# Optimization experiments

Measured on AMD Instinct MI355X. Metric: run time of the kernel, lower is better.

Reference implementation:

```python
import jax, jax.numpy as jnp
import numpy as np

N_USERS = 1_000_000
AVG_DEG = 32
E = N_USERS * AVG_DEG
K = 5
IN_F = 1
OUT_F = 64
BN_EPS = 1e-5


def setup_inputs() -> dict:
    key = jax.random.key(0)
    ks = jax.random.split(key, 6)
    stdv = 1.0 / np.sqrt(IN_F * K)
    return {
        "x": jax.random.normal(ks[0], (N_USERS, IN_F), dtype=jnp.float32),
        "edge_index": jax.random.randint(ks[1], (2, E), 0, N_USERS, dtype=jnp.int32),
        "edge_weight": jax.random.uniform(ks[2], (E,), dtype=jnp.float32),
        "weight": jax.random.uniform(ks[3], (OUT_F, K, IN_F), dtype=jnp.float32, minval=-stdv, maxval=stdv),
        "bias": jax.random.uniform(ks[4], (OUT_F,), dtype=jnp.float32, minval=-stdv, maxval=stdv),
        "gamma": jnp.ones((N_USERS,), dtype=jnp.float32),
        "beta": jnp.zeros((N_USERS,), dtype=jnp.float32),
    }


def reference(x, edge_index, edge_weight, weight, bias, gamma, beta):
    N = x.shape[0]
    src, dst = edge_index[0], edge_index[1]
    # K-hop propagation: gather x_j, scale by edge_weight, scatter-add at dst
    feats = [x]
    cur = x
    for _ in range(K - 1):
        msg = cur[src] * edge_weight[:, None]                 # [E, IN_F]
        cur = jax.ops.segment_sum(msg, dst, num_segments=N)   # [N, IN_F]
        feats.append(cur)
    # [N, K*IN_F], hop-major / feature-minor ordering (matches torch reshape)
    conv = jnp.concatenate(feats, axis=1)[None]               # [1, N, K*IN_F]
    h = weight.reshape(OUT_F, K * IN_F).T                     # [K*IN_F, OUT_F]
    y = jnp.matmul(conv, h) + bias                            # [1, N, OUT_F]
    # BatchNorm1d(N_users) in training mode: stats over (batch, feature) per node-channel
    mean = jnp.mean(y, axis=(0, 2), keepdims=True)
    var = jnp.mean((y - mean) ** 2, axis=(0, 2), keepdims=True)  # biased var
    y_hat = (y - mean) * jax.lax.rsqrt(var + BN_EPS)
    return y_hat * gamma[None, :, None] + beta[None, :, None]
```

## Files before the change

### kernel.cpp

```cpp
#include <hip/hip_runtime.h>

#define N_USERS 1000000
#define NEDGE   32000000
#define OUT_F   64
#define BN_EPS  1e-5f

#define SBITS     12
#define S_BUCKET  4096
#define NB        245
#define CAP       139264
#define SCAT_BLOCKS 1024
#define CHUNK     (NEDGE / SCAT_BLOCKS)
#define SPLIT     8

typedef unsigned int uint4v __attribute__((ext_vector_type(4)));


__global__ void init_cursors(unsigned* __restrict__ cursors) {
    int i = blockIdx.x * blockDim.x + threadIdx.x;
    if (i < NB) cursors[i] = (unsigned)i * CAP;
}

__global__ __launch_bounds__(256) void scatter_bin(
    const int* __restrict__ src, const int* __restrict__ dst,
    const float* __restrict__ ew, uint2* __restrict__ rec,
    unsigned* __restrict__ cursors) {
    __shared__ unsigned cnt[NB];
    __shared__ unsigned base[NB];
    int tid = threadIdx.x;
    int start = blockIdx.x * CHUNK;
    int end = start + CHUNK;

    for (int i = tid; i < NB; i += 256) cnt[i] = 0;
    __syncthreads();
    for (int i = start + tid; i < end; i += 256) {
        int d = __builtin_nontemporal_load(&dst[i]);
        atomicAdd(&cnt[d >> SBITS], 1u);
    }
    __syncthreads();
    for (int i = tid; i < NB; i += 256) {
        unsigned c = cnt[i];
        base[i] = c ? atomicAdd(&cursors[i], c) : 0u;
    }
    __syncthreads();
    for (int i = tid; i < NB; i += 256) cnt[i] = 0;
    __syncthreads();
    for (int i = start + tid; i < end; i += 256) {
        int d = __builtin_nontemporal_load(&dst[i]);
        int s = __builtin_nontemporal_load(&src[i]);
        float w = __builtin_nontemporal_load(&ew[i]);
        int b = d >> SBITS;
        unsigned p = base[b] + atomicAdd(&cnt[b], 1u);
        unsigned meta = ((unsigned)(d & (S_BUCKET - 1)) << 20) | (unsigned)s;
        rec[p] = make_uint2(meta, __float_as_uint(w));
    }
}

__global__ __launch_bounds__(256) void hop_bucket_split(
    const uint2* __restrict__ rec, const unsigned* __restrict__ cursors,
    const float* __restrict__ cur, float* __restrict__ nxt) {
    __shared__ float acc[S_BUCKET];
    int tid = threadIdx.x;
    int b = blockIdx.x / SPLIT;
    int s = blockIdx.x % SPLIT;
    for (int i = tid; i < S_BUCKET; i += 256) acc[i] = 0.0f;
    __syncthreads();

    unsigned start = (unsigned)b * CAP;
    unsigned cnt = cursors[b] - start;
    unsigned u0 = ((cnt * (unsigned)s) / SPLIT) & ~3u;
    unsigned u1 = (s == SPLIT - 1) ? cnt : (((cnt * (unsigned)(s + 1)) / SPLIT) & ~3u);
    const uint2* bptr = rec + start;

    unsigned i = u0 + 4u * (unsigned)tid;
    for (; i + 4u <= u1; i += 4u * 256u) {
        uint4v r0 = __builtin_nontemporal_load(reinterpret_cast<const uint4v*>(bptr + i));
        uint4v r1 = __builtin_nontemporal_load(reinterpret_cast<const uint4v*>(bptr + i + 2));
        float c0 = cur[r0.x & 0xFFFFFu];
        float c1 = cur[r0.z & 0xFFFFFu];
        float c2 = cur[r1.x & 0xFFFFFu];
        float c3 = cur[r1.z & 0xFFFFFu];
        atomicAdd(&acc[r0.x >> 20], c0 * __uint_as_float(r0.y));
        atomicAdd(&acc[r0.z >> 20], c1 * __uint_as_float(r0.w));
        atomicAdd(&acc[r1.x >> 20], c2 * __uint_as_float(r1.y));
        atomicAdd(&acc[r1.z >> 20], c3 * __uint_as_float(r1.w));
    }
    if (i < u1) {
        for (unsigned j = i; j < i + 4u && j < u1; ++j) {
            uint2 r = bptr[j];
            atomicAdd(&acc[r.x >> 20], cur[r.x & 0xFFFFFu] * __uint_as_float(r.y));
        }
    }
    __syncthreads();

    int nb0 = b << SBITS;
    for (int k = tid; k < S_BUCKET; k += 256) {
        int n = nb0 + k;
        if (n < N_USERS) atomicAdd(&nxt[n], acc[k]);
    }
}


__global__ void zero_kernel(float* __restrict__ p, int n) {
    int i = blockIdx.x * blockDim.x + threadIdx.x;
    int stride = gridDim.x * blockDim.x;
    for (; i < n; i += stride) p[i] = 0.0f;
}

__global__ __launch_bounds__(256) void hop_atomic(
    const int* __restrict__ src, const int* __restrict__ dst,
    const float* __restrict__ ew, const float* __restrict__ cur,
    float* __restrict__ nxt) {
    int e = blockIdx.x * blockDim.x + threadIdx.x;
    if (e * 4 < NEDGE) {
        int4   s = ((const int4*)src)[e];
        int4   d = ((const int4*)dst)[e];
        float4 w = ((const float4*)ew)[e];
        atomicAdd(&nxt[d.x], cur[s.x] * w.x);
        atomicAdd(&nxt[d.y], cur[s.y] * w.y);
        atomicAdd(&nxt[d.z], cur[s.z] * w.z);
        atomicAdd(&nxt[d.w], cur[s.w] * w.w);
    }
}


__global__ __launch_bounds__(256) void finalize_kernel(
    const float* __restrict__ x,  const float* __restrict__ f1,
    const float* __restrict__ f2, const float* __restrict__ f3,
    const float* __restrict__ f4, const float* __restrict__ W,
    const float* __restrict__ bias, const float* __restrict__ gamma,
    const float* __restrict__ beta, float* __restrict__ out) {
    int lane = threadIdx.x & 63;
    int waveInBlock = threadIdx.x >> 6;
    int wavesPerBlock = blockDim.x >> 6;
    int gwave  = blockIdx.x * wavesPerBlock + waveInBlock;
    int nwaves = gridDim.x * wavesPerBlock;

    float w0 = W[lane * 5 + 0];
    float w1 = W[lane * 5 + 1];
    float w2 = W[lane * 5 + 2];
    float w3 = W[lane * 5 + 3];
    float w4 = W[lane * 5 + 4];
    float b  = bias[lane];

    for (int n = gwave; n < N_USERS; n += nwaves) {
        float c0 = x[n], c1 = f1[n], c2 = f2[n], c3 = f3[n], c4 = f4[n];
        float y = b + c0 * w0 + c1 * w1 + c2 * w2 + c3 * w3 + c4 * w4;

        float s = y;
        #pragma unroll
        for (int off = 32; off; off >>= 1) s += __shfl_xor(s, off);
        float mean = s * (1.0f / 64.0f);

        float d = y - mean;
        float v = d * d;
        #pragma unroll
        for (int off = 32; off; off >>= 1) v += __shfl_xor(v, off);
        float var = v * (1.0f / 64.0f);

        float o = d * rsqrtf(var + BN_EPS) * gamma[n] + beta[n];
        __builtin_nontemporal_store(o, &out[(size_t)n * OUT_F + lane]);
    }
}

extern "C" void kernel_launch(void* const* d_in, const int* in_sizes, int n_in,
                              void* d_out, int out_size, void* d_ws, size_t ws_size,
                              hipStream_t stream) {
    const float* x     = (const float*)d_in[0];
    const int*   ei    = (const int*)d_in[1];
    const float* ew    = (const float*)d_in[2];
    const float* W     = (const float*)d_in[3];
    const float* bias  = (const float*)d_in[4];
    const float* gamma = (const float*)d_in[5];
    const float* beta  = (const float*)d_in[6];
    float* out = (float*)d_out;

    const int* src = ei;
    const int* dst = ei + NEDGE;

    float* f = (float*)d_ws;
    uint2* rec = (uint2*)(f + 4ull * N_USERS);
    unsigned* cursors = (unsigned*)(rec + (size_t)NB * CAP);
    size_t needed = 4ull * N_USERS * 4 + (size_t)NB * CAP * 8 + (size_t)NB * 4;

    if (ws_size >= needed) {
        init_cursors<<<1, 256, 0, stream>>>(cursors);
        zero_kernel<<<2048, 256, 0, stream>>>(f, 4 * N_USERS);
        scatter_bin<<<SCAT_BLOCKS, 256, 0, stream>>>(src, dst, ew, rec, cursors);
        const float* cur = x;
        for (int h = 0; h < 4; ++h) {
            float* nxt = f + (size_t)h * N_USERS;
            hop_bucket_split<<<NB * SPLIT, 256, 0, stream>>>(rec, cursors, cur, nxt);
            cur = nxt;
        }
    } else {
        zero_kernel<<<4096, 256, 0, stream>>>(f, 4 * N_USERS);
        const float* cur = x;
        for (int h = 0; h < 4; ++h) {
            float* nxt = f + (size_t)h * N_USERS;
            hop_atomic<<<NEDGE / 4 / 256, 256, 0, stream>>>(src, dst, ew, cur, nxt);
            cur = nxt;
        }
    }

    finalize_kernel<<<2048, 256, 0, stream>>>(
        x, f, f + N_USERS, f + 2 * N_USERS, f + 3 * N_USERS,
        W, bias, gamma, beta, out);
}
```

Baseline: 1.917 ms.

## Sort binned edges into per-node CSR and run hops as atomic-free row gathers

Adds a one-time sort_bucket pass that counting-sorts each destination bucket's edge records into a per-node CSR layout (rowstart, plus a one-byte rowcnt). Each hop then becomes a one-thread-per-node gather with no shared or global atomics, and the per-hop zeroing is dropped. The sorted records are staged in the output buffer as scratch space. Risks: only 64 blocks do the sort, and the guard requires out_size to hold NB*CAP*8 bytes. That exceeds the 256 MB output, so the slower global-atomic fallback path may run instead.

```diff
diff --git a/kernel.cpp b/kernel.cpp
--- a/kernel.cpp
+++ b/kernel.cpp
@@ -8,10 +8,10 @@
 #define SBITS     12
 #define S_BUCKET  4096
 #define NB        245
-#define CAP       139264
+#define CAP       136896
 #define SCAT_BLOCKS 1024
 #define CHUNK     (NEDGE / SCAT_BLOCKS)
-#define SPLIT     8
+#define SORT_BLOCKS 64
 
 typedef unsigned int uint4v __attribute__((ext_vector_type(4)));
 
@@ -56,48 +56,114 @@
     }
 }
 
-__global__ __launch_bounds__(256) void hop_bucket_split(
+__global__ __launch_bounds__(256) void sort_bucket(
     const uint2* __restrict__ rec, const unsigned* __restrict__ cursors,
-    const float* __restrict__ cur, float* __restrict__ nxt) {
-    __shared__ float acc[S_BUCKET];
+    uint2* __restrict__ rec2, unsigned* __restrict__ rowstart,
+    unsigned char* __restrict__ rowcnt) {
+    __shared__ unsigned offs[S_BUCKET];
+    __shared__ unsigned cnt2[S_BUCKET];
+    __shared__ unsigned chunkT[256];
     int tid = threadIdx.x;
-    int b = blockIdx.x / SPLIT;
-    int s = blockIdx.x % SPLIT;
-    for (int i = tid; i < S_BUCKET; i += 256) acc[i] = 0.0f;
-    __syncthreads();
-
-    unsigned start = (unsigned)b * CAP;
-    unsigned cnt = cursors[b] - start;
-    unsigned u0 = ((cnt * (unsigned)s) / SPLIT) & ~3u;
-    unsigned u1 = (s == SPLIT - 1) ? cnt : (((cnt * (unsigned)(s + 1)) / SPLIT) & ~3u);
-    const uint2* bptr = rec + start;
-
-    unsigned i = u0 + 4u * (unsigned)tid;
-    for (; i + 4u <= u1; i += 4u * 256u) {
-        uint4v r0 = __builtin_nontemporal_load(reinterpret_cast<const uint4v*>(bptr + i));
-        uint4v r1 = __builtin_nontemporal_load(reinterpret_cast<const uint4v*>(bptr + i + 2));
-        float c0 = cur[r0.x & 0xFFFFFu];
-        float c1 = cur[r0.z & 0xFFFFFu];
-        float c2 = cur[r1.x & 0xFFFFFu];
-        float c3 = cur[r1.z & 0xFFFFFu];
-        atomicAdd(&acc[r0.x >> 20], c0 * __uint_as_float(r0.y));
-        atomicAdd(&acc[r0.z >> 20], c1 * __uint_as_float(r0.w));
-        atomicAdd(&acc[r1.x >> 20], c2 * __uint_as_float(r1.y));
-        atomicAdd(&acc[r1.z >> 20], c3 * __uint_as_float(r1.w));
-    }
-    if (i < u1) {
-        for (unsigned j = i; j < i + 4u && j < u1; ++j) {
-            uint2 r = bptr[j];
-            atomicAdd(&acc[r.x >> 20], cur[r.x & 0xFFFFFu] * __uint_as_float(r.y));
-        }
-    }
-    __syncthreads();
-
-    int nb0 = b << SBITS;
-    for (int k = tid; k < S_BUCKET; k += 256) {
-        int n = nb0 + k;
-        if (n < N_USERS) atomicAdd(&nxt[n], acc[k]);
-    }
+
+    for (int b = blockIdx.x; b < NB; b += SORT_BLOCKS) {
+        for (int k = tid; k < S_BUCKET; k += 256) { offs[k] = 0; cnt2[k] = 0; }
+        __syncthreads();
+
+        unsigned start = (unsigned)b * CAP;
+        unsigned n = cursors[b] - start;
+        const uint2* bp = rec + start;
+
+        unsigned i = 2u * (unsigned)tid;
+        for (; i + 2u <= n; i += 512u) {
+            uint4v r = __builtin_nontemporal_load(reinterpret_cast<const uint4v*>(bp + i));
+            atomicAdd(&offs[r.x >> 20], 1u);
+            atomicAdd(&offs[r.z >> 20], 1u);
+        }
+        if (i < n) {
+            uint2 r = bp[i];
+            atomicAdd(&offs[r.x >> 20], 1u);
+        }
+        __syncthreads();
+
+        int nb0 = b << SBITS;
+        for (int k = tid; k < S_BUCKET; k += 256)
+            rowcnt[nb0 + k] = (unsigned char)offs[k];
+        __syncthreads();
+
+        {
+            int base = tid * 16;
+            unsigned run = 0;
+            for (int k = 0; k < 16; ++k) { unsigned v = offs[base + k]; offs[base + k] = run; run += v; }
+            chunkT[tid] = run;
+        }
+        __syncthreads();
+        if (tid == 0) {
+            unsigned run = 0;
+            for (int t = 0; t < 256; ++t) { unsigned v = chunkT[t]; chunkT[t] = run; run += v; }
+        }
+        __syncthreads();
+        {
+            int base = tid * 16;
+            unsigned add = chunkT[tid];
+            for (int k = 0; k < 16; ++k) offs[base + k] += add;
+        }
+        __syncthreads();
+
+        for (int k = tid; k < S_BUCKET; k += 256)
+            rowstart[nb0 + k] = start + offs[k];
+
+        i = 2u * (unsigned)tid;
+        for (; i + 2u <= n; i += 512u) {
+            uint4v r = __builtin_nontemporal_load(reinterpret_cast<const uint4v*>(bp + i));
+            unsigned d0 = r.x >> 20, d1 = r.z >> 20;
+            unsigned p0 = offs[d0] + atomicAdd(&cnt2[d0], 1u);
+            unsigned p1 = offs[d1] + atomicAdd(&cnt2[d1], 1u);
+            rec2[start + p0] = make_uint2(r.x & 0xFFFFFu, r.y);
+            rec2[start + p1] = make_uint2(r.z & 0xFFFFFu, r.w);
+        }
+        if (i < n) {
+            uint2 r = bp[i];
+            unsigned d0 = r.x >> 20;
+            unsigned p0 = offs[d0] + atomicAdd(&cnt2[d0], 1u);
+            rec2[start + p0] = make_uint2(r.x & 0xFFFFFu, r.y);
+        }
+        __syncthreads();
+    }
+}
+
+__global__ __launch_bounds__(256) void hop_csr(
+    const uint2* __restrict__ rec2, const unsigned* __restrict__ rowstart,
+    const unsigned char* __restrict__ rowcnt, const float* __restrict__ cur,
+    float* __restrict__ nxt) {
+    int n = blockIdx.x * 256 + threadIdx.x;
+    if (n >= N_USERS) return;
+    unsigned s = rowstart[n];
+    int c = rowcnt[n];
+    float sum = 0.0f;
+    if ((s & 1u) && c > 0) {
+        uint2 r = rec2[s];
+        sum += cur[r.x] * __uint_as_float(r.y);
+        ++s; --c;
+    }
+    for (; c >= 4; c -= 4, s += 4) {
+        uint4v r0 = __builtin_nontemporal_load(reinterpret_cast<const uint4v*>(rec2 + s));
+        uint4v r1 = __builtin_nontemporal_load(reinterpret_cast<const uint4v*>(rec2 + s + 2));
+        float c0 = cur[r0.x], c1 = cur[r0.z], c2 = cur[r1.x], c3 = cur[r1.z];
+        sum += c0 * __uint_as_float(r0.y);
+        sum += c1 * __uint_as_float(r0.w);
+        sum += c2 * __uint_as_float(r1.y);
+        sum += c3 * __uint_as_float(r1.w);
+    }
+    for (; c >= 2; c -= 2, s += 2) {
+        uint4v r = __builtin_nontemporal_load(reinterpret_cast<const uint4v*>(rec2 + s));
+        sum += cur[r.x] * __uint_as_float(r.y);
+        sum += cur[r.z] * __uint_as_float(r.w);
+    }
+    if (c) {
+        uint2 r = rec2[s];
+        sum += cur[r.x] * __uint_as_float(r.y);
+    }
+    nxt[n] = sum;
 }
 
 
@@ -181,16 +247,21 @@
     float* f = (float*)d_ws;
     uint2* rec = (uint2*)(f + 4ull * N_USERS);
     unsigned* cursors = (unsigned*)(rec + (size_t)NB * CAP);
-    size_t needed = 4ull * N_USERS * 4 + (size_t)NB * CAP * 8 + (size_t)NB * 4;
-
-    if (ws_size >= needed) {
+    unsigned* rowstart = cursors + 1024;
+    unsigned char* rowcnt = (unsigned char*)(rowstart + (size_t)NB * S_BUCKET);
+    size_t needed = 16000000ull + (size_t)NB * CAP * 8 + 4096
+                  + (size_t)NB * S_BUCKET * 4 + (size_t)NB * S_BUCKET;
+
+    uint2* rec2 = (uint2*)d_out;
+
+    if (ws_size >= needed && (size_t)out_size >= (size_t)NB * CAP * 8) {
         init_cursors<<<1, 256, 0, stream>>>(cursors);
-        zero_kernel<<<2048, 256, 0, stream>>>(f, 4 * N_USERS);
         scatter_bin<<<SCAT_BLOCKS, 256, 0, stream>>>(src, dst, ew, rec, cursors);
+        sort_bucket<<<SORT_BLOCKS, 256, 0, stream>>>(rec, cursors, rec2, rowstart, rowcnt);
         const float* cur = x;
         for (int h = 0; h < 4; ++h) {
             float* nxt = f + (size_t)h * N_USERS;
-            hop_bucket_split<<<NB * SPLIT, 256, 0, stream>>>(rec, cursors, cur, nxt);
+            hop_csr<<<(N_USERS + 255) / 256, 256, 0, stream>>>(rec2, rowstart, rowcnt, cur, nxt);
             cur = nxt;
         }
     } else {
```

Result: slower. 6.674 ms (+248.1%).

## Stage binning in shared memory per tile and write bucket runs contiguously

Applied to the files above, without the earlier changes.

The scatter-binning kernel now processes 4096-edge tiles. Each tile is sorted by bucket in LDS using a local histogram and a prefix sum, and is then copied to the global bucket array in runs, so global stores become mostly contiguous instead of scattered per edge. Dst indices are held in registers so they are read once rather than twice. The per-bucket capacity is reduced slightly. This adds a serial single-thread prefix sum, more LDS use (about 45KB, which limits occupancy) and more global cursor atomics per tile. It also risks overflowing a bucket if its real count exceeds the smaller CAP.

```diff
diff --git a/kernel.cpp b/kernel.cpp
--- a/kernel.cpp
+++ b/kernel.cpp
@@ -8,9 +8,10 @@
 #define SBITS     12
 #define S_BUCKET  4096
 #define NB        245
-#define CAP       139264
+#define CAP       136896
 #define SCAT_BLOCKS 1024
-#define CHUNK     (NEDGE / SCAT_BLOCKS)
+#define TILE      4096
+#define NTILES    ((NEDGE + TILE - 1) / TILE)
 #define SPLIT     8
 
 typedef unsigned int uint4v __attribute__((ext_vector_type(4)));
@@ -25,57 +26,90 @@
     const int* __restrict__ src, const int* __restrict__ dst,
     const float* __restrict__ ew, uint2* __restrict__ rec,
     unsigned* __restrict__ cursors) {
-    __shared__ unsigned cnt[NB];
-    __shared__ unsigned base[NB];
+    __shared__ uint2 srec[TILE];
+    __shared__ unsigned short sbkt[TILE];
+    __shared__ unsigned hist[NB];
+    __shared__ unsigned curs[NB];
+    __shared__ unsigned gpos[NB];
     int tid = threadIdx.x;
-    int start = blockIdx.x * CHUNK;
-    int end = start + CHUNK;
-
-    for (int i = tid; i < NB; i += 256) cnt[i] = 0;
-    __syncthreads();
-    for (int i = start + tid; i < end; i += 256) {
-        int d = __builtin_nontemporal_load(&dst[i]);
-        atomicAdd(&cnt[d >> SBITS], 1u);
-    }
-    __syncthreads();
-    for (int i = tid; i < NB; i += 256) {
-        unsigned c = cnt[i];
-        base[i] = c ? atomicAdd(&cursors[i], c) : 0u;
-    }
-    __syncthreads();
-    for (int i = tid; i < NB; i += 256) cnt[i] = 0;
-    __syncthreads();
-    for (int i = start + tid; i < end; i += 256) {
-        int d = __builtin_nontemporal_load(&dst[i]);
-        int s = __builtin_nontemporal_load(&src[i]);
-        float w = __builtin_nontemporal_load(&ew[i]);
-        int b = d >> SBITS;
-        unsigned p = base[b] + atomicAdd(&cnt[b], 1u);
-        unsigned meta = ((unsigned)(d & (S_BUCKET - 1)) << 20) | (unsigned)s;
-        rec[p] = make_uint2(meta, __float_as_uint(w));
-    }
-}
-
-__global__ __launch_bounds__(256) void hop_bucket_split(
+
+    for (int tile = blockIdx.x; tile < NTILES; tile += gridDim.x) {
+        int e0 = tile * TILE;
+        int n_this = (e0 + TILE <= NEDGE) ? TILE : (NEDGE - e0);
+
+        for (int i = tid; i < NB; i += 256) hist[i] = 0;
+        __syncthreads();
+
+        int d[16];
+        #pragma unroll
+        for (int k = 0; k < 16; ++k) {
+            int e = e0 + k * 256 + tid;
+            if (e < NEDGE) {
+                d[k] = __builtin_nontemporal_load(&dst[e]);
+                atomicAdd(&hist[d[k] >> SBITS], 1u);
+            }
+        }
+        __syncthreads();
+
+        if (tid == 0) {
+            unsigned run = 0;
+            for (int b = 0; b < NB; ++b) { unsigned v = hist[b]; hist[b] = run; run += v; }
+        }
+        __syncthreads();
+
+        for (int b = tid; b < NB; b += 256) {
+            unsigned st = hist[b];
+            unsigned en = (b == NB - 1) ? (unsigned)n_this : hist[b + 1];
+            unsigned c = en - st;
+            gpos[b] = c ? atomicAdd(&cursors[b], c) : 0u;
+            curs[b] = 0;
+        }
+        __syncthreads();
+
+        #pragma unroll
+        for (int k = 0; k < 16; ++k) {
+            int e = e0 + k * 256 + tid;
+            if (e < NEDGE) {
+                int dd = d[k];
+                int b = dd >> SBITS;
+                int s = __builtin_nontemporal_load(&src[e]);
+                float w = __builtin_nontemporal_load(&ew[e]);
+                unsigned p = hist[b] + atomicAdd(&curs[b], 1u);
+                srec[p] = make_uint2(((unsigned)(dd & (S_BUCKET - 1)) << 20) | (unsigned)s,
+                                     __float_as_uint(w));
+                sbkt[p] = (unsigned short)b;
+            }
+        }
+        __syncthreads();
+
+        for (int i = tid; i < n_this; i += 256) {
+            unsigned b = sbkt[i];
+            rec[gpos[b] + ((unsigned)i - hist[b])] = srec[i];
+        }
+        __syncthreads();
+    }
+}
+
+__global__ __launch_bounds__(256) void hop_bucket(
     const uint2* __restrict__ rec, const unsigned* __restrict__ cursors,
     const float* __restrict__ cur, float* __restrict__ nxt) {
     __shared__ float acc[S_BUCKET];
     int tid = threadIdx.x;
     int b = blockIdx.x / SPLIT;
-    int s = blockIdx.x % SPLIT;
+    int sidx = blockIdx.x % SPLIT;
     for (int i = tid; i < S_BUCKET; i += 256) acc[i] = 0.0f;
     __syncthreads();
 
     unsigned start = (unsigned)b * CAP;
     unsigned cnt = cursors[b] - start;
-    unsigned u0 = ((cnt * (unsigned)s) / SPLIT) & ~3u;
-    unsigned u1 = (s == SPLIT - 1) ? cnt : (((cnt * (unsigned)(s + 1)) / SPLIT) & ~3u);
-    const uint2* bptr = rec + start;
+    unsigned u0 = ((cnt * (unsigned)sidx) / SPLIT) & ~3u;
+    unsigned u1 = (sidx == SPLIT - 1) ? cnt : (((cnt * (unsigned)(sidx + 1)) / SPLIT) & ~3u);
+    const uint2* bp = rec + start;
 
     unsigned i = u0 + 4u * (unsigned)tid;
     for (; i + 4u <= u1; i += 4u * 256u) {
-        uint4v r0 = __builtin_nontemporal_load(reinterpret_cast<const uint4v*>(bptr + i));
-        uint4v r1 = __builtin_nontemporal_load(reinterpret_cast<const uint4v*>(bptr + i + 2));
+        uint4v r0 = __builtin_nontemporal_load(reinterpret_cast<const uint4v*>(bp + i));
+        uint4v r1 = __builtin_nontemporal_load(reinterpret_cast<const uint4v*>(bp + i + 2));
         float c0 = cur[r0.x & 0xFFFFFu];
         float c1 = cur[r0.z & 0xFFFFFu];
         float c2 = cur[r1.x & 0xFFFFFu];
@@ -87,7 +121,7 @@
     }
     if (i < u1) {
         for (unsigned j = i; j < i + 4u && j < u1; ++j) {
-            uint2 r = bptr[j];
+            uint2 r = bp[j];
             atomicAdd(&acc[r.x >> 20], cur[r.x & 0xFFFFFu] * __uint_as_float(r.y));
         }
     }
@@ -181,7 +215,7 @@
     float* f = (float*)d_ws;
     uint2* rec = (uint2*)(f + 4ull * N_USERS);
     unsigned* cursors = (unsigned*)(rec + (size_t)NB * CAP);
-    size_t needed = 4ull * N_USERS * 4 + (size_t)NB * CAP * 8 + (size_t)NB * 4;
+    size_t needed = 16000000ull + (size_t)NB * CAP * 8 + 4096;
 
     if (ws_size >= needed) {
         init_cursors<<<1, 256, 0, stream>>>(cursors);
@@ -190,7 +224,7 @@
         const float* cur = x;
         for (int h = 0; h < 4; ++h) {
             float* nxt = f + (size_t)h * N_USERS;
-            hop_bucket_split<<<NB * SPLIT, 256, 0, stream>>>(rec, cursors, cur, nxt);
+            hop_bucket<<<NB * SPLIT, 256, 0, stream>>>(rec, cursors, cur, nxt);
             cur = nxt;
         }
     } else {
```

Measured after the change: 1.781 ms. -7.1%, faster.
